# Performance work log

Measured on AMD Instinct MI355X. Metric: run time of the kernel, lower is better.

Reference implementation:

```python
import jax, jax.numpy as jnp
import numpy as np

NUM_LAYERS = 4
D_MODEL = 512
D_INNER = 1024   # 2 * d_model (Mamba expand=2)
D_STATE = 16
DT_RANK = 32     # ceil(d_model / 16)
D_CONV = 4
BATCH = 2
SEQ = 512
EPS = 1e-5


def _rmsnorm(x, w, eps=EPS):
    # fused add+RMSNorm math: fp32 reduction, scale by weight (no bias)
    x = x.astype(jnp.float32)
    return x * jax.lax.rsqrt(jnp.mean(x * x, axis=-1, keepdims=True) + eps) * w


def _silu(x):
    return x * jax.nn.sigmoid(x)


def _causal_conv(x, w, b):
    # x: (B, D, L); w: (D, K) depthwise causal conv, left-pad K-1, take first L
    xp = jnp.pad(x, ((0, 0), (0, 0), (D_CONV - 1, 0)))
    out = jax.lax.conv_general_dilated(
        xp, w[:, None, :], (1,), 'VALID',
        dimension_numbers=('NCH', 'OIH', 'NCH'),
        feature_group_count=x.shape[1])
    return out + b[None, :, None]


def _selective_scan(u, delta, A, Bm, Cm):
    # u, delta: (B, D, L); A: (D, N); Bm, Cm: (B, N, L)
    xs = (jnp.moveaxis(delta, 2, 0), jnp.moveaxis(u, 2, 0),
          jnp.moveaxis(Bm, 2, 0), jnp.moveaxis(Cm, 2, 0))
    h0 = jnp.zeros((u.shape[0], u.shape[1], A.shape[1]), u.dtype)

    def step(h, xst):
        d_t, u_t, b_t, c_t = xst                     # (B,D),(B,D),(B,N),(B,N)
        dA = jnp.exp(d_t[:, :, None] * A[None])      # (B,D,N) ZOH discretization
        h = h * dA + (d_t * u_t)[:, :, None] * b_t[:, None, :]
        y = jnp.einsum('bdn,bn->bd', h, c_t)
        return h, y

    _, ys = jax.lax.scan(step, h0, xs)
    return jnp.moveaxis(ys, 0, 2)                    # (B, D, L)


def _ssm_branch(x, z, cw, cb, xpw, dtw, dtb, Alog, Dskip):
    x = _silu(_causal_conv(x, cw, cb))                              # (B, Din, L)
    x_dbl = jnp.einsum('rd,bdl->brl', xpw, x)                       # (B, R+2N, L)
    dt, Bm, Cm = jnp.split(x_dbl, [DT_RANK, DT_RANK + D_STATE], axis=1)
    delta = jax.nn.softplus(jnp.einsum('dr,brl->bdl', dtw, dt) + dtb[None, :, None])
    A = -jnp.exp(Alog.astype(jnp.float32))                          # (Din, N)
    y = _selective_scan(x, delta, A, Bm, Cm)
    y = y + Dskip[None, :, None] * x
    return y * _silu(z)


def _encoder(x, norm_w, in_proj_w, convw_f, convb_f, xpw_f, dtw_f, dtb_f,
             Alog_f, Dskip_f, convw_r, convb_r, xpw_r, dtw_r, dtb_r,
             Alog_r, Dskip_r, out_proj_w, normf_w):
    residual = None
    hs = x
    feats = []
    for i in range(NUM_LAYERS):
        # fused add + RMSNorm, prenorm=True, residual_in_fp32
        residual = hs if residual is None else (hs + residual)
        residual = residual.astype(jnp.float32)
        hn = _rmsnorm(residual, norm_w[i])
        # bimamba v2 mixer
        xz = jnp.einsum('ed,bld->bel', in_proj_w[i], hn)            # (B, 2Din, L)
        xi, zi = jnp.split(xz, 2, axis=1)
        y_f = _ssm_branch(xi, zi, convw_f[i], convb_f[i], xpw_f[i], dtw_f[i],
                          dtb_f[i], Alog_f[i], Dskip_f[i])
        y_r = _ssm_branch(xi[:, :, ::-1], zi[:, :, ::-1], convw_r[i], convb_r[i],
                          xpw_r[i], dtw_r[i], dtb_r[i], Alog_r[i], Dskip_r[i])
        y = y_f + y_r[:, :, ::-1]
        hs = jnp.einsum('bel,de->bld', y, out_proj_w[i])
        feats.append(hs)
    out = _rmsnorm(hs + residual, normf_w)                          # prenorm=False
    return out, feats


def setup_inputs() -> dict:
    key = jax.random.key(0)
    ks = jax.random.split(key, 12)
    Ly = NUM_LAYERS
    s = 0.02

    def nrm(k, shape):
        return jax.random.normal(k, shape, jnp.float32) * s

    dt = 1e-3 + jax.random.uniform(ks[11], (Ly, D_INNER), jnp.float32) * (0.1 - 1e-3)
    dtb = jnp.log(jnp.expm1(dt))  # inverse softplus of dt init
    Alog = jnp.log(jnp.broadcast_to(
        jnp.arange(1, D_STATE + 1, dtype=jnp.float32), (Ly, D_INNER, D_STATE)))
    return dict(
        x=jax.random.normal(ks[0], (BATCH, SEQ, D_MODEL), jnp.float32),
        norm_w=jnp.ones((Ly, D_MODEL), jnp.float32),
        in_proj_w=nrm(ks[1], (Ly, 2 * D_INNER, D_MODEL)),
        convw_f=nrm(ks[2], (Ly, D_INNER, D_CONV)),
        convb_f=jnp.zeros((Ly, D_INNER), jnp.float32),
        xpw_f=nrm(ks[3], (Ly, DT_RANK + 2 * D_STATE, D_INNER)),
        dtw_f=nrm(ks[4], (Ly, D_INNER, DT_RANK)),
        dtb_f=dtb,
        Alog_f=Alog,
        Dskip_f=jnp.ones((Ly, D_INNER), jnp.float32),
        convw_r=nrm(ks[5], (Ly, D_INNER, D_CONV)),
        convb_r=jnp.zeros((Ly, D_INNER), jnp.float32),
        xpw_r=nrm(ks[6], (Ly, DT_RANK + 2 * D_STATE, D_INNER)),
        dtw_r=nrm(ks[7], (Ly, D_INNER, DT_RANK)),
        dtb_r=dtb,
        Alog_r=Alog,
        Dskip_r=jnp.ones((Ly, D_INNER), jnp.float32),
        out_proj_w=nrm(ks[8], (Ly, D_MODEL, D_INNER)),
        normf_w=jnp.ones((D_MODEL,), jnp.float32),
    )


def reference(x, norm_w, in_proj_w, convw_f, convb_f, xpw_f, dtw_f, dtb_f,
              Alog_f, Dskip_f, convw_r, convb_r, xpw_r, dtw_r, dtb_r,
              Alog_r, Dskip_r, out_proj_w, normf_w):
    out, feats = _encoder(x, norm_w, in_proj_w, convw_f, convb_f, xpw_f, dtw_f,
                          dtb_f, Alog_f, Dskip_f, convw_r, convb_r, xpw_r,
                          dtw_r, dtb_r, Alog_r, Dskip_r, out_proj_w, normf_w)
    return (out, jnp.stack(feats))
```

## Files before the change

### kernel.cpp

```cpp
#include <hip/hip_runtime.h>

#define BATCH 2
#define SEQ 512
#define DMODEL 512
#define DINNER 1024
#define DSTATE 16
#define DTRANK 32
#define NBL (BATCH*SEQ)
#define EPSV 1e-5f

typedef __attribute__((ext_vector_type(8))) short bf16x8;
typedef __attribute__((ext_vector_type(4))) float f32x4;

static __device__ __forceinline__ float sigmoidf_(float x) {
  return 1.0f / (1.0f + __expf(-x));
}
static __device__ __forceinline__ float softplusf_(float x) {
  return fmaxf(x, 0.0f) + log1pf(__expf(-fabsf(x)));
}
static __device__ __forceinline__ unsigned short f2bf(float x) {
  unsigned int u = __float_as_uint(x);
  unsigned int r = (u + 0x7FFFu + ((u >> 16) & 1u)) >> 16;
  return (unsigned short)r;
}
static __device__ __forceinline__ float bf2f(short s) {
  return __uint_as_float(((unsigned int)(unsigned short)s) << 16);
}

__global__ __launch_bounds__(256) void wconvert_kernel(
    const float* __restrict__ s0, const float* __restrict__ s1,
    const float* __restrict__ s2, const float* __restrict__ s3,
    const float* __restrict__ s4, const float* __restrict__ s5,
    unsigned short* __restrict__ d0, unsigned short* __restrict__ d1,
    unsigned short* __restrict__ d2, unsigned short* __restrict__ d3,
    unsigned short* __restrict__ d4, unsigned short* __restrict__ d5) {
  long i = (long)(blockIdx.x * 256 + threadIdx.x) * 8;
  const float* src; unsigned short* dst;
  if (i < 4194304)      { src = s0; dst = d0; }
  else if (i < 6291456) { src = s1; dst = d1; i -= 4194304; }
  else if (i < 6553600) { src = s2; dst = d2; i -= 6291456; }
  else if (i < 6815744) { src = s3; dst = d3; i -= 6553600; }
  else if (i < 6946816) { src = s4; dst = d4; i -= 6815744; }
  else                  { src = s5; dst = d5; i -= 6946816; }
  const float4 v0 = *(const float4*)&src[i];
  const float4 v1 = *(const float4*)&src[i + 4];
  bf16x8 o;
  o[0] = (short)f2bf(v0.x); o[1] = (short)f2bf(v0.y);
  o[2] = (short)f2bf(v0.z); o[3] = (short)f2bf(v0.w);
  o[4] = (short)f2bf(v1.x); o[5] = (short)f2bf(v1.y);
  o[6] = (short)f2bf(v1.z); o[7] = (short)f2bf(v1.w);
  *(bf16x8*)&dst[i] = o;
}

__global__ __launch_bounds__(256) void addnorm_kernel(
    const float* __restrict__ hs, float* __restrict__ residual,
    const float* __restrict__ w, float* __restrict__ out,
    unsigned short* __restrict__ outb, int first) {
  const int row = blockIdx.x;
  const int t = threadIdx.x;
  const float* hp = hs + (long)row * DMODEL;
  float* rp = residual + (long)row * DMODEL;
  float r0 = hp[t], r1 = hp[t + 256];
  if (!first) { r0 += rp[t]; r1 += rp[t + 256]; }
  rp[t] = r0; rp[t + 256] = r1;
  float ss = r0 * r0 + r1 * r1;
  #pragma unroll
  for (int off = 32; off; off >>= 1) ss += __shfl_xor(ss, off, 64);
  __shared__ float sw[4];
  const int wid = t >> 6, lane = t & 63;
  if (lane == 0) sw[wid] = ss;
  __syncthreads();
  const float tot = sw[0] + sw[1] + sw[2] + sw[3];
  const float scale = rsqrtf(tot * (1.0f / (float)DMODEL) + EPSV);
  const float v0 = r0 * scale * w[t];
  const float v1 = r1 * scale * w[t + 256];
  if (out) {
    out[(long)row * DMODEL + t] = v0;
    out[(long)row * DMODEL + t + 256] = v1;
  }
  if (outb) {
    outb[(long)row * DMODEL + t] = f2bf(v0);
    outb[(long)row * DMODEL + t + 256] = f2bf(v1);
  }
}

#define LDK2 72

__global__ __launch_bounds__(256) void gemm_in_kernel(
    const unsigned short* __restrict__ A, const unsigned short* __restrict__ B,
    float* __restrict__ C) {
  __shared__ unsigned short As[128 * LDK2];
  __shared__ unsigned short Bs[64 * LDK2];
  const int t = threadIdx.x;
  const int m0 = blockIdx.y * 128, n0 = blockIdx.x * 64;
  const int lane = t & 63;
  const int w = t >> 6;
  const int wr = (w >> 1) * 64, wc = (w & 1) * 32;
  const int fr = lane & 15;
  const int fq = lane >> 4;
  const int K = DMODEL;

  f32x4 acc[4][2];
  #pragma unroll
  for (int i = 0; i < 4; ++i)
    #pragma unroll
    for (int j = 0; j < 2; ++j) {
      f32x4 z = {0.f, 0.f, 0.f, 0.f};
      acc[i][j] = z;
    }

  const int arow = t >> 1, ako = (t & 1) * 32;
  const int brow = t >> 2, bko = (t & 3) * 16;

  bf16x8 pa[4], pb[2];
  #define LOADG_IN(k0_) do {                                              \
    const unsigned short* ap = &A[(long)(m0 + arow) * K + (k0_) + ako];   \
    pa[0] = *(const bf16x8*)ap;        pa[1] = *(const bf16x8*)(ap + 8);  \
    pa[2] = *(const bf16x8*)(ap + 16); pa[3] = *(const bf16x8*)(ap + 24); \
    const unsigned short* bp = &B[(long)(n0 + brow) * K + (k0_) + bko];   \
    pb[0] = *(const bf16x8*)bp;        pb[1] = *(const bf16x8*)(bp + 8);  \
  } while (0)

  LOADG_IN(0);
  for (int k0 = 0; k0 < K; k0 += 64) {
    if (k0) __syncthreads();
    *(bf16x8*)&As[arow * LDK2 + ako]      = pa[0];
    *(bf16x8*)&As[arow * LDK2 + ako + 8]  = pa[1];
    *(bf16x8*)&As[arow * LDK2 + ako + 16] = pa[2];
    *(bf16x8*)&As[arow * LDK2 + ako + 24] = pa[3];
    *(bf16x8*)&Bs[brow * LDK2 + bko]      = pb[0];
    *(bf16x8*)&Bs[brow * LDK2 + bko + 8]  = pb[1];
    __syncthreads();
    if (k0 + 64 < K) LOADG_IN(k0 + 64);
    #pragma unroll
    for (int h = 0; h < 2; ++h) {
      bf16x8 af[4], bg[2];
      #pragma unroll
      for (int i = 0; i < 4; ++i)
        af[i] = *(const bf16x8*)&As[(wr + i * 16 + fr) * LDK2 + h * 32 + fq * 8];
      #pragma unroll
      for (int j = 0; j < 2; ++j)
        bg[j] = *(const bf16x8*)&Bs[(wc + j * 16 + fr) * LDK2 + h * 32 + fq * 8];
      #pragma unroll
      for (int i = 0; i < 4; ++i)
        #pragma unroll
        for (int j = 0; j < 2; ++j)
          acc[i][j] = __builtin_amdgcn_mfma_f32_16x16x32_bf16(
              af[i], bg[j], acc[i][j], 0, 0, 0);
    }
  }
  #undef LOADG_IN

  #pragma unroll
  for (int i = 0; i < 4; ++i)
    #pragma unroll
    for (int j = 0; j < 2; ++j)
      #pragma unroll
      for (int r2 = 0; r2 < 4; ++r2) {
        const int m = m0 + wr + i * 16 + fq * 4 + r2;
        const int n = n0 + wc + j * 16 + fr;
        C[(long)m * NBL + n] = acc[i][j][r2];
      }
}

__global__ __launch_bounds__(256) void conv_silu_kernel(
    const float* __restrict__ xz,
    const float* __restrict__ cw_f, const float* __restrict__ cb_f,
    const float* __restrict__ cw_r, const float* __restrict__ cb_r,
    unsigned short* __restrict__ xcT) {
  __shared__ unsigned short tile[32][33];
  const int dir = blockIdx.z;
  const int n0 = blockIdx.x * 32, d0 = blockIdx.y * 32;
  const int b = n0 >> 9;
  const int l0 = n0 & (SEQ - 1);
  const float* cw = dir ? cw_r : cw_f;
  const float* cb = dir ? cb_r : cb_f;
  unsigned short* dst = xcT + (long)dir * DINNER * NBL;
  const int t = threadIdx.x;
  const int c = t & 31, rr = t >> 5;
  #pragma unroll
  for (int p = 0; p < 4; ++p) {
    const int d = d0 + p * 8 + rr;
    const int l = l0 + c;
    const float* xi = xz + (long)d * NBL + b * SEQ;
    float sum = cb[d];
    #pragma unroll
    for (int k = 0; k < 4; ++k) {
      const int tt = l - 3 + k;
      if (tt >= 0) {
        const int src = dir ? (SEQ - 1 - tt) : tt;
        sum += cw[d * 4 + k] * xi[src];
      }
    }
    const float v = sum * sigmoidf_(sum);
    tile[p * 8 + rr][c] = f2bf(v);
  }
  __syncthreads();
  #pragma unroll
  for (int p = 0; p < 4; ++p) {
    const int n = n0 + p * 8 + rr;
    dst[(long)n * DINNER + d0 + c] = tile[c][p * 8 + rr];
  }
}

__global__ __launch_bounds__(256) void xdbl_mfma_kernel(
    const unsigned short* __restrict__ xpwb_f, const unsigned short* __restrict__ xpwb_r,
    const unsigned short* __restrict__ xcT,
    unsigned short* __restrict__ dtT,
    float* __restrict__ xbc_f, float* __restrict__ xbc_r) {
  __shared__ unsigned short As[64 * LDK2];
  __shared__ unsigned short Bs[32 * LDK2];
  const int t = threadIdx.x;
  const int dir = blockIdx.y;
  const int n0 = blockIdx.x * 32;
  const unsigned short* A = dir ? xpwb_r : xpwb_f;
  const unsigned short* B = xcT + (long)dir * DINNER * NBL;
  float* xbc = dir ? xbc_r : xbc_f;
  unsigned short* dtt = dtT + (long)dir * NBL * DTRANK;

  const int lane = t & 63;
  const int w = t >> 6;
  const int wr = (w >> 1) * 32, wc = (w & 1) * 16;
  const int fr = lane & 15;
  const int fq = lane >> 4;

  f32x4 acc[2];
  #pragma unroll
  for (int i = 0; i < 2; ++i) {
    f32x4 z = {0.f, 0.f, 0.f, 0.f};
    acc[i] = z;
  }

  const int arow = t >> 2, ako = (t & 3) * 16;
  const int brow = t >> 3, bko = (t & 7) * 8;

  bf16x8 pa[2], pb;
  #define LOADG_XD(k0_) do {                                                   \
    const unsigned short* ap = &A[(long)arow * DINNER + (k0_) + ako];          \
    pa[0] = *(const bf16x8*)ap;        pa[1] = *(const bf16x8*)(ap + 8);       \
    pb = *(const bf16x8*)&B[(long)(n0 + brow) * DINNER + (k0_) + bko];         \
  } while (0)

  LOADG_XD(0);
  for (int k0 = 0; k0 < DINNER; k0 += 64) {
    if (k0) __syncthreads();
    *(bf16x8*)&As[arow * LDK2 + ako]     = pa[0];
    *(bf16x8*)&As[arow * LDK2 + ako + 8] = pa[1];
    *(bf16x8*)&Bs[brow * LDK2 + bko]     = pb;
    __syncthreads();
    if (k0 + 64 < DINNER) LOADG_XD(k0 + 64);
    #pragma unroll
    for (int h = 0; h < 2; ++h) {
      bf16x8 af[2], bg;
      #pragma unroll
      for (int i = 0; i < 2; ++i)
        af[i] = *(const bf16x8*)&As[(wr + i * 16 + fr) * LDK2 + h * 32 + fq * 8];
      bg = *(const bf16x8*)&Bs[(wc + fr) * LDK2 + h * 32 + fq * 8];
      #pragma unroll
      for (int i = 0; i < 2; ++i)
        acc[i] = __builtin_amdgcn_mfma_f32_16x16x32_bf16(af[i], bg, acc[i], 0, 0, 0);
    }
  }
  #undef LOADG_XD

  #pragma unroll
  for (int i = 0; i < 2; ++i)
    #pragma unroll
    for (int r2 = 0; r2 < 4; ++r2) {
      const int m = wr + i * 16 + fq * 4 + r2;
      const int n = n0 + wc + fr;
      const float v = acc[i][r2];
      if (m < DTRANK) dtt[(long)n * DTRANK + m] = f2bf(v);
      else xbc[(long)(m - 32) * NBL + n] = v;
    }
}

static __device__ __forceinline__ void scan_pass(
    const float dt[8], const float u[8],
    const float* __restrict__ bct, const float* __restrict__ Alog,
    float Dv, int lane, float out[8]) {
  float dtu[8];
  #pragma unroll
  for (int j = 0; j < 8; ++j) { dtu[j] = dt[j] * u[j]; out[j] = 0.f; }
  const float dts = ((dt[0] + dt[1]) + (dt[2] + dt[3])) +
                    ((dt[4] + dt[5]) + (dt[6] + dt[7]));

  for (int n = 0; n < DSTATE; ++n) {
    const float An = -__expf(Alog[n]);
    float Bv[8], Cv[8], dA[8], cB[8];
    {
      const float* bp = bct + (long)n * NBL;
      const float* cp = bct + (long)(DSTATE + n) * NBL;
      const float4 b0 = *(const float4*)&bp[0];
      const float4 b1 = *(const float4*)&bp[4];
      Bv[0] = b0.x; Bv[1] = b0.y; Bv[2] = b0.z; Bv[3] = b0.w;
      Bv[4] = b1.x; Bv[5] = b1.y; Bv[6] = b1.z; Bv[7] = b1.w;
      const float4 c0 = *(const float4*)&cp[0];
      const float4 c1 = *(const float4*)&cp[4];
      Cv[0] = c0.x; Cv[1] = c0.y; Cv[2] = c0.z; Cv[3] = c0.w;
      Cv[4] = c1.x; Cv[5] = c1.y; Cv[6] = c1.z; Cv[7] = c1.w;
    }
    float h = 0.f;
    #pragma unroll
    for (int j = 0; j < 8; ++j) {
      dA[j] = __expf(dt[j] * An);
      cB[j] = dtu[j] * Bv[j];
      h = fmaf(h, dA[j], cB[j]);
    }
    const float P = __expf(dts * An);
    float hs = h, Ps = P;
    #pragma unroll
    for (int off = 1; off < 64; off <<= 1) {
      const float hp = __shfl_up(hs, off, 64);
      const float Pp = __shfl_up(Ps, off, 64);
      if (lane >= off) { hs = fmaf(hp, Ps, hs); Ps *= Pp; }
    }
    float h0 = __shfl_up(hs, 1, 64);
    if (lane == 0) h0 = 0.f;
    #pragma unroll
    for (int j = 0; j < 8; ++j) {
      h0 = fmaf(h0, dA[j], cB[j]);
      out[j] = fmaf(h0, Cv[j], out[j]);
    }
  }
  #pragma unroll
  for (int j = 0; j < 8; ++j) out[j] = fmaf(Dv, u[j], out[j]);
}

__global__ __launch_bounds__(512) void scan_split_kernel(
    const unsigned short* __restrict__ dtT,
    const unsigned short* __restrict__ dtwb_f, const unsigned short* __restrict__ dtwb_r,
    const float* __restrict__ dtb_f, const float* __restrict__ dtb_r,
    const float* __restrict__ xbc_f, const float* __restrict__ xbc_r,
    const float* __restrict__ Alog_f, const float* __restrict__ Alog_r,
    const float* __restrict__ Dsk_f, const float* __restrict__ Dsk_r,
    const float* __restrict__ cw_f, const float* __restrict__ cb_f,
    const float* __restrict__ cw_r, const float* __restrict__ cb_r,
    const float* __restrict__ xz, unsigned short* __restrict__ ybt) {
  __shared__ float s_r[4][2][256];
  __shared__ unsigned short s_y[4][512];
  const int t = threadIdx.x;
  const int wv = t >> 6;
  const int lane = t & 63;
  const int dir = wv & 1;
  const int dl = wv >> 1;
  const int row = blockIdx.x * 4 + dl;
  const int b = row >> 10, d = row & 1023;
  const long rbase = (long)d * NBL + b * SEQ;

  float xv[8];
  {
    const float* xp = xz + rbase + lane * 8;
    const float4 a0 = *(const float4*)&xp[0];
    const float4 a1 = *(const float4*)&xp[4];
    xv[0] = a0.x; xv[1] = a0.y; xv[2] = a0.z; xv[3] = a0.w;
    xv[4] = a1.x; xv[5] = a1.y; xv[6] = a1.z; xv[7] = a1.w;
  }
  if (dir) {
    float xr[8];
    #pragma unroll
    for (int j = 0; j < 8; ++j) xr[j] = __shfl(xv[7 - j], 63 - lane, 64);
    #pragma unroll
    for (int j = 0; j < 8; ++j) xv[j] = xr[j];
  }
  const float* cwp = dir ? cw_r : cw_f;
  const float* cbp = dir ? cb_r : cb_f;
  float u[8];
  {
    const float cw0 = cwp[d * 4], cw1 = cwp[d * 4 + 1], cw2 = cwp[d * 4 + 2],
                cw3 = cwp[d * 4 + 3], cb = cbp[d];
    const float xm1 = __shfl_up(xv[7], 1, 64);
    const float xm2 = __shfl_up(xv[6], 1, 64);
    const float xm3 = __shfl_up(xv[5], 1, 64);
    const float ext[3] = {xm3, xm2, xm1};
    #pragma unroll
    for (int j = 0; j < 8; ++j) {
      float s = cb + cw3 * xv[j];
      const int p = lane * 8 + j;
      #pragma unroll
      for (int k = 0; k < 3; ++k) {
        const int idx = j - 3 + k;
        const float xval = (idx >= 0) ? xv[idx] : ext[3 + idx];
        if (p - 3 + k >= 0) s += (k == 0 ? cw0 : (k == 1 ? cw1 : cw2)) * xval;
      }
      u[j] = s * sigmoidf_(s);
    }
  }

  float dtv[8];
  {
    const unsigned short* dw = ((dir ? dtwb_r : dtwb_f)) + (long)d * DTRANK;
    float w32[32];
    #pragma unroll
    for (int q = 0; q < 4; ++q) {
      const bf16x8 v = *(const bf16x8*)&dw[q * 8];
      #pragma unroll
      for (int e = 0; e < 8; ++e) w32[q * 8 + e] = bf2f(v[e]);
    }
    const float bias = (dir ? dtb_r : dtb_f)[d];
    const unsigned short* dtrow =
        dtT + (long)dir * NBL * DTRANK + ((long)b * SEQ + lane * 8) * DTRANK;
    #pragma unroll
    for (int j = 0; j < 8; ++j) {
      const bf16x8* rp = (const bf16x8*)&dtrow[(long)j * DTRANK];
      float acc = bias;
      #pragma unroll
      for (int q = 0; q < 4; ++q) {
        const bf16x8 rv = rp[q];
        #pragma unroll
        for (int e = 0; e < 8; ++e)
          acc = fmaf(w32[q * 8 + e], bf2f(rv[e]), acc);
      }
      dtv[j] = softplusf_(acc);
    }
  }

  float a[8];
  scan_pass(dtv, u,
            (dir ? xbc_r : xbc_f) + b * SEQ + lane * 8,
            (dir ? Alog_r : Alog_f) + d * DSTATE,
            (dir ? Dsk_r : Dsk_f)[d], lane, a);

  if (dir) {
    float fv[8];
    #pragma unroll
    for (int j = 0; j < 8; ++j) fv[j] = __shfl(a[7 - j], 63 - lane, 64);
    float4 q0 = {fv[0], fv[1], fv[2], fv[3]};
    float4 q1 = {fv[4], fv[5], fv[6], fv[7]};
    *(float4*)&s_r[dl][0][lane * 4] = q0;
    *(float4*)&s_r[dl][1][lane * 4] = q1;
  }
  __syncthreads();
  if (!dir) {
    const float* zp = xz + (long)(DINNER + d) * NBL + b * SEQ + lane * 8;
    const float4 z0 = *(const float4*)&zp[0];
    const float4 z1 = *(const float4*)&zp[4];
    const float zv[8] = {z0.x, z0.y, z0.z, z0.w, z1.x, z1.y, z1.z, z1.w};
    const float4 r0 = *(const float4*)&s_r[dl][0][lane * 4];
    const float4 r1 = *(const float4*)&s_r[dl][1][lane * 4];
    const float rr[8] = {r0.x, r0.y, r0.z, r0.w, r1.x, r1.y, r1.z, r1.w};
    bf16x8 ob;
    #pragma unroll
    for (int j = 0; j < 8; ++j) {
      const float tot = a[j] + rr[j];
      ob[j] = (short)f2bf(tot * (zv[j] * sigmoidf_(zv[j])));
    }
    *(bf16x8*)&s_y[dl][lane * 8] = ob;
  }
  __syncthreads();
  const int d0 = (blockIdx.x * 4) & 1023;
  const int bb = (blockIdx.x * 4) >> 10;
  unsigned short* yrow = ybt + (long)(bb * SEQ) * DINNER + d0;
  {
    const int n = t;
    ushort4 v = {s_y[0][n], s_y[1][n], s_y[2][n], s_y[3][n]};
    *(ushort4*)&yrow[(long)n * DINNER] = v;
  }
}

__global__ __launch_bounds__(256) void gemm_out_kernel(
    const unsigned short* __restrict__ A, const unsigned short* __restrict__ B,
    float* __restrict__ C) {
  __shared__ unsigned short As[64 * LDK2];
  __shared__ unsigned short Bs[64 * LDK2];
  const int t = threadIdx.x;
  const int m0 = blockIdx.y * 64, n0 = blockIdx.x * 64;
  const int lane = t & 63;
  const int w = t >> 6;
  const int wr = (w >> 1) * 32, wc = (w & 1) * 32;
  const int fr = lane & 15;
  const int fq = lane >> 4;
  const int K = DINNER;

  f32x4 acc[2][2];
  #pragma unroll
  for (int i = 0; i < 2; ++i)
    #pragma unroll
    for (int j = 0; j < 2; ++j) {
      f32x4 z = {0.f, 0.f, 0.f, 0.f};
      acc[i][j] = z;
    }

  const int arow = t >> 2, ako = (t & 3) * 16;

  bf16x8 pa[2], pb[2];
  #define LOADG_OUT(k0_) do {                                              \
    const unsigned short* ap = &A[(long)(m0 + arow) * K + (k0_) + ako];    \
    pa[0] = *(const bf16x8*)ap;        pa[1] = *(const bf16x8*)(ap + 8);   \
    const unsigned short* bp = &B[(long)(n0 + arow) * K + (k0_) + ako];    \
    pb[0] = *(const bf16x8*)bp;        pb[1] = *(const bf16x8*)(bp + 8);   \
  } while (0)

  LOADG_OUT(0);
  for (int k0 = 0; k0 < K; k0 += 64) {
    if (k0) __syncthreads();
    *(bf16x8*)&As[arow * LDK2 + ako]     = pa[0];
    *(bf16x8*)&As[arow * LDK2 + ako + 8] = pa[1];
    *(bf16x8*)&Bs[arow * LDK2 + ako]     = pb[0];
    *(bf16x8*)&Bs[arow * LDK2 + ako + 8] = pb[1];
    __syncthreads();
    if (k0 + 64 < K) LOADG_OUT(k0 + 64);
    #pragma unroll
    for (int h = 0; h < 2; ++h) {
      bf16x8 af[2], bg[2];
      #pragma unroll
      for (int i = 0; i < 2; ++i) {
        af[i] = *(const bf16x8*)&As[(wr + i * 16 + fr) * LDK2 + h * 32 + fq * 8];
        bg[i] = *(const bf16x8*)&Bs[(wc + i * 16 + fr) * LDK2 + h * 32 + fq * 8];
      }
      #pragma unroll
      for (int i = 0; i < 2; ++i)
        #pragma unroll
        for (int j = 0; j < 2; ++j)
          acc[i][j] = __builtin_amdgcn_mfma_f32_16x16x32_bf16(
              af[i], bg[j], acc[i][j], 0, 0, 0);
    }
  }
  #undef LOADG_OUT

  #pragma unroll
  for (int i = 0; i < 2; ++i)
    #pragma unroll
    for (int j = 0; j < 2; ++j)
      #pragma unroll
      for (int r2 = 0; r2 < 4; ++r2) {
        const int m = m0 + wr + i * 16 + fq * 4 + r2;
        const int n = n0 + wc + j * 16 + fr;
        C[(long)n * DMODEL + m] = acc[i][j][r2];
      }
}

extern "C" void kernel_launch(void* const* d_in, const int* in_sizes, int n_in,
                              void* d_out, int out_size, void* d_ws, size_t ws_size,
                              hipStream_t stream) {
  (void)in_sizes; (void)n_in; (void)out_size; (void)ws_size;
  const float* x       = (const float*)d_in[0];
  const float* norm_w  = (const float*)d_in[1];
  const float* in_proj = (const float*)d_in[2];
  const float* convw_f = (const float*)d_in[3];
  const float* convb_f = (const float*)d_in[4];
  const float* xpw_f   = (const float*)d_in[5];
  const float* dtw_f   = (const float*)d_in[6];
  const float* dtb_f   = (const float*)d_in[7];
  const float* Alog_f  = (const float*)d_in[8];
  const float* Dsk_f   = (const float*)d_in[9];
  const float* convw_r = (const float*)d_in[10];
  const float* convb_r = (const float*)d_in[11];
  const float* xpw_r   = (const float*)d_in[12];
  const float* dtw_r   = (const float*)d_in[13];
  const float* dtb_r   = (const float*)d_in[14];
  const float* Alog_r  = (const float*)d_in[15];
  const float* Dsk_r   = (const float*)d_in[16];
  const float* out_w   = (const float*)d_in[17];
  const float* normf_w = (const float*)d_in[18];

  float* ws = (float*)d_ws;
  float* residual = ws;  ws += 524288;
  float* xzbuf    = ws;  ws += 2097152;
  float* xbc_f    = ws;  ws += 32768;
  float* xbc_r    = ws;  ws += 32768;
  float* hnb_f    = ws;  ws += 262144;
  float* wbfin_f  = ws;  ws += 2097152;
  float* wbfout_f = ws;  ws += 1048576;
  float* ybt_f    = ws;  ws += 524288;
  float* xcT_f    = ws;  ws += 1048576;
  float* dtT_f    = ws;  ws += 32768;
  float* xpwb_f_  = ws;  ws += 131072;
  float* xpwb_r_  = ws;  ws += 131072;
  float* dtwb_f_  = ws;  ws += 65536;
  float* dtwb_r_  = ws;  ws += 65536;

  unsigned short* hnb = (unsigned short*)hnb_f;
  unsigned short* wbfin = (unsigned short*)wbfin_f;
  unsigned short* wbfout = (unsigned short*)wbfout_f;
  unsigned short* ybt = (unsigned short*)ybt_f;
  unsigned short* xcT = (unsigned short*)xcT_f;
  unsigned short* dtT = (unsigned short*)dtT_f;
  unsigned short* xpwb_f = (unsigned short*)xpwb_f_;
  unsigned short* xpwb_r = (unsigned short*)xpwb_r_;
  unsigned short* dtwb_f = (unsigned short*)dtwb_f_;
  unsigned short* dtwb_r = (unsigned short*)dtwb_r_;

  float* outp = (float*)d_out;

  wconvert_kernel<<<3456, 256, 0, stream>>>(
      in_proj, out_w, xpw_f, xpw_r, dtw_f, dtw_r,
      wbfin, wbfout, xpwb_f, xpwb_r, dtwb_f, dtwb_r);

  for (int layer = 0; layer < 4; ++layer) {
    const float* hsrc = layer == 0 ? x : (outp + (long)layer * 524288);
    addnorm_kernel<<<1024, 256, 0, stream>>>(
        hsrc, residual, norm_w + layer * DMODEL, nullptr, hnb, layer == 0 ? 1 : 0);
    gemm_in_kernel<<<dim3(16, 16), 256, 0, stream>>>(
        wbfin + (long)layer * 2048 * 512, hnb, xzbuf);
    conv_silu_kernel<<<dim3(32, 32, 2), 256, 0, stream>>>(
        xzbuf, convw_f + layer * DINNER * 4, convb_f + layer * DINNER,
        convw_r + layer * DINNER * 4, convb_r + layer * DINNER, xcT);
    xdbl_mfma_kernel<<<dim3(32, 2), 256, 0, stream>>>(
        xpwb_f + (long)layer * 64 * DINNER, xpwb_r + (long)layer * 64 * DINNER,
        xcT, dtT, xbc_f, xbc_r);
    scan_split_kernel<<<512, 512, 0, stream>>>(
        dtT, dtwb_f + (long)layer * DINNER * DTRANK,
        dtwb_r + (long)layer * DINNER * DTRANK,
        dtb_f + layer * DINNER, dtb_r + layer * DINNER,
        xbc_f, xbc_r,
        Alog_f + layer * DINNER * DSTATE, Alog_r + layer * DINNER * DSTATE,
        Dsk_f + layer * DINNER, Dsk_r + layer * DINNER,
        convw_f + layer * DINNER * 4, convb_f + layer * DINNER,
        convw_r + layer * DINNER * 4, convb_r + layer * DINNER,
        xzbuf, ybt);
    gemm_out_kernel<<<dim3(16, 8), 256, 0, stream>>>(
        wbfout + (long)layer * 512 * 1024, ybt,
        outp + (long)(1 + layer) * 524288);
  }
  addnorm_kernel<<<1024, 256, 0, stream>>>(
      outp + 4 * 524288, residual, normf_w, outp, nullptr, 0);
}
```

Measured before the change: 317.0 us.

## Replace shuffle-based wavefront scan with DPP row scan plus readlane combine

The 64-lane inclusive scan in the selective-scan kernel now uses DPP row_shr within each 16-lane row, then combines the rows with readlane broadcasts, replacing six rounds of ds_bpermute-based shfl_up. The dt low-rank intermediate is also stored in fp32 instead of bf16, which doubles its buffer size and the bytes the scan kernel reads. The DPP path avoids LDS-routed shuffles on the serial scan critical path, at the cost of more intricate masking logic. Keeping dt in fp32 also improves accuracy.

```diff
diff --git a/kernel.cpp b/kernel.cpp
--- a/kernel.cpp
+++ b/kernel.cpp
@@ -25,6 +25,21 @@
 }
 static __device__ __forceinline__ float bf2f(short s) {
   return __uint_as_float(((unsigned int)(unsigned short)s) << 16);
+}
+static __device__ __forceinline__ float dpp_shr(float v, int ctrl) {
+  switch (ctrl) {
+    case 1: return __int_as_float(__builtin_amdgcn_update_dpp(
+        0, __float_as_int(v), 0x111, 0xf, 0xf, true));
+    case 2: return __int_as_float(__builtin_amdgcn_update_dpp(
+        0, __float_as_int(v), 0x112, 0xf, 0xf, true));
+    case 4: return __int_as_float(__builtin_amdgcn_update_dpp(
+        0, __float_as_int(v), 0x114, 0xf, 0xf, true));
+    default: return __int_as_float(__builtin_amdgcn_update_dpp(
+        0, __float_as_int(v), 0x118, 0xf, 0xf, true));
+  }
+}
+static __device__ __forceinline__ float rdlane(float v, int l) {
+  return __int_as_float(__builtin_amdgcn_readlane(__float_as_int(v), l));
 }
 
 __global__ __launch_bounds__(256) void wconvert_kernel(
@@ -206,7 +221,7 @@
 __global__ __launch_bounds__(256) void xdbl_mfma_kernel(
     const unsigned short* __restrict__ xpwb_f, const unsigned short* __restrict__ xpwb_r,
     const unsigned short* __restrict__ xcT,
-    unsigned short* __restrict__ dtT,
+    float* __restrict__ dtT,
     float* __restrict__ xbc_f, float* __restrict__ xbc_r) {
   __shared__ unsigned short As[64 * LDK2];
   __shared__ unsigned short Bs[32 * LDK2];
@@ -216,7 +231,7 @@
   const unsigned short* A = dir ? xpwb_r : xpwb_f;
   const unsigned short* B = xcT + (long)dir * DINNER * NBL;
   float* xbc = dir ? xbc_r : xbc_f;
-  unsigned short* dtt = dtT + (long)dir * NBL * DTRANK;
+  float* dtt = dtT + (long)dir * NBL * DTRANK;
 
   const int lane = t & 63;
   const int w = t >> 6;
@@ -270,7 +285,7 @@
       const int m = wr + i * 16 + fq * 4 + r2;
       const int n = n0 + wc + fr;
       const float v = acc[i][r2];
-      if (m < DTRANK) dtt[(long)n * DTRANK + m] = f2bf(v);
+      if (m < DTRANK) dtt[(long)n * DTRANK + m] = v;
       else xbc[(long)(m - 32) * NBL + n] = v;
     }
 }
@@ -284,6 +299,12 @@
   for (int j = 0; j < 8; ++j) { dtu[j] = dt[j] * u[j]; out[j] = 0.f; }
   const float dts = ((dt[0] + dt[1]) + (dt[2] + dt[3])) +
                     ((dt[4] + dt[5]) + (dt[6] + dt[7]));
+  const int lr = lane & 15;
+  const int rowi = lane >> 4;
+  const float m1 = (lr < 1) ? 1.f : 0.f;
+  const float m2 = (lr < 2) ? 1.f : 0.f;
+  const float m4 = (lr < 4) ? 1.f : 0.f;
+  const float m8 = (lr < 8) ? 1.f : 0.f;
 
   for (int n = 0; n < DSTATE; ++n) {
     const float An = -__expf(Alog[n]);
@@ -307,16 +328,28 @@
       cB[j] = dtu[j] * Bv[j];
       h = fmaf(h, dA[j], cB[j]);
     }
-    const float P = __expf(dts * An);
-    float hs = h, Ps = P;
-    #pragma unroll
-    for (int off = 1; off < 64; off <<= 1) {
-      const float hp = __shfl_up(hs, off, 64);
-      const float Pp = __shfl_up(Ps, off, 64);
-      if (lane >= off) { hs = fmaf(hp, Ps, hs); Ps *= Pp; }
-    }
-    float h0 = __shfl_up(hs, 1, 64);
-    if (lane == 0) h0 = 0.f;
+    float hs = h, Ps = __expf(dts * An);
+    {
+      float hp, Pp;
+      hp = dpp_shr(hs, 1); Pp = dpp_shr(Ps, 1);
+      hs = fmaf(hp, Ps, hs); Ps *= (Pp + m1);
+      hp = dpp_shr(hs, 2); Pp = dpp_shr(Ps, 2);
+      hs = fmaf(hp, Ps, hs); Ps *= (Pp + m2);
+      hp = dpp_shr(hs, 4); Pp = dpp_shr(Ps, 4);
+      hs = fmaf(hp, Ps, hs); Ps *= (Pp + m4);
+      hp = dpp_shr(hs, 8); Pp = dpp_shr(Ps, 8);
+      hs = fmaf(hp, Ps, hs); Ps *= (Pp + m8);
+    }
+    const float Th0 = rdlane(hs, 15), Tp0 = rdlane(Ps, 15);
+    const float Th1 = rdlane(hs, 31), Tp1 = rdlane(Ps, 31);
+    const float Th2 = rdlane(hs, 47), Tp2 = rdlane(Ps, 47);
+    const float c2h = fmaf(Th0, Tp1, Th1);
+    const float c3h = fmaf(c2h, Tp2, Th2);
+    const float Ch = (rowi == 0) ? 0.f : (rowi == 1) ? Th0
+                     : (rowi == 2) ? c2h : c3h;
+    const float H = fmaf(Ch, Ps, hs);
+    float h0 = dpp_shr(H, 1);
+    if (lr == 0) h0 = Ch;
     #pragma unroll
     for (int j = 0; j < 8; ++j) {
       h0 = fmaf(h0, dA[j], cB[j]);
@@ -328,7 +361,7 @@
 }
 
 __global__ __launch_bounds__(512) void scan_split_kernel(
-    const unsigned short* __restrict__ dtT,
+    const float* __restrict__ dtT,
     const unsigned short* __restrict__ dtwb_f, const unsigned short* __restrict__ dtwb_r,
     const float* __restrict__ dtb_f, const float* __restrict__ dtb_r,
     const float* __restrict__ xbc_f, const float* __restrict__ xbc_r,
@@ -398,18 +431,19 @@
       for (int e = 0; e < 8; ++e) w32[q * 8 + e] = bf2f(v[e]);
     }
     const float bias = (dir ? dtb_r : dtb_f)[d];
-    const unsigned short* dtrow =
+    const float* dtrow =
         dtT + (long)dir * NBL * DTRANK + ((long)b * SEQ + lane * 8) * DTRANK;
     #pragma unroll
     for (int j = 0; j < 8; ++j) {
-      const bf16x8* rp = (const bf16x8*)&dtrow[(long)j * DTRANK];
+      const float4* rp = (const float4*)&dtrow[(long)j * DTRANK];
       float acc = bias;
       #pragma unroll
-      for (int q = 0; q < 4; ++q) {
-        const bf16x8 rv = rp[q];
-        #pragma unroll
-        for (int e = 0; e < 8; ++e)
-          acc = fmaf(w32[q * 8 + e], bf2f(rv[e]), acc);
+      for (int q = 0; q < 8; ++q) {
+        const float4 rv = rp[q];
+        acc = fmaf(w32[q * 4 + 0], rv.x, acc);
+        acc = fmaf(w32[q * 4 + 1], rv.y, acc);
+        acc = fmaf(w32[q * 4 + 2], rv.z, acc);
+        acc = fmaf(w32[q * 4 + 3], rv.w, acc);
       }
       dtv[j] = softplusf_(acc);
     }
@@ -564,7 +598,7 @@
   float* wbfout_f = ws;  ws += 1048576;
   float* ybt_f    = ws;  ws += 524288;
   float* xcT_f    = ws;  ws += 1048576;
-  float* dtT_f    = ws;  ws += 32768;
+  float* dtT     = ws;  ws += 65536;
   float* xpwb_f_  = ws;  ws += 131072;
   float* xpwb_r_  = ws;  ws += 131072;
   float* dtwb_f_  = ws;  ws += 65536;
@@ -575,7 +609,6 @@
   unsigned short* wbfout = (unsigned short*)wbfout_f;
   unsigned short* ybt = (unsigned short*)ybt_f;
   unsigned short* xcT = (unsigned short*)xcT_f;
-  unsigned short* dtT = (unsigned short*)dtT_f;
   unsigned short* xpwb_f = (unsigned short*)xpwb_f_;
   unsigned short* xpwb_r = (unsigned short*)xpwb_r_;
   unsigned short* dtwb_f = (unsigned short*)dtwb_f_;
```

Measured after the change: 417.1 us. 31.6% more time.
